# Kernel optimization log

Measured on AMD Instinct MI355X. Metric: run time of the kernel, lower is better.

The kernel has to match this reference:

```python
import jax, jax.numpy as jnp
import numpy as np

TEMPERATURE = 10.0  # module init temperature (training mode)


def setup_inputs() -> dict:
    key = jax.random.key(0)
    kx, kg = jax.random.split(key)
    B, C, H, W = 64, 128, 64, 64
    n = C * H * W  # 524288
    x = jax.random.normal(kx, (B, C, H, W), dtype=jnp.float32)
    # Gumbel(0,1) noise for Gumbel-top-k sampling (== multinomial w/o replacement)
    u = jax.random.uniform(kg, (B, n), dtype=jnp.float32, minval=1e-20, maxval=1.0)
    gumbel = -jnp.log(-jnp.log(u))
    k = int(round(0.1 * n))  # percent_on * n = 52429
    return {"x": x, "gumbel": gumbel, "k": k}


def reference(x, gumbel, k):
    B = x.shape[0]
    n = x.shape[1] * x.shape[2] * x.shape[3]
    flat = x.reshape(B, n)                      # [B, n]
    logits = flat / TEMPERATURE
    # Categorical sampling of k winners without replacement == top-k of
    # gumbel-perturbed logits (equivalent to softmax(logits) + multinomial).
    _, idx = jax.lax.top_k(logits + gumbel, k)  # [B, k]
    mask = jnp.zeros((B, n), dtype=x.dtype).at[jnp.arange(B)[:, None], idx].set(1.0)
    out = (flat * mask).reshape(x.shape)
    return jnp.maximum(out, 0.0)  # relu=True
```

## Files before the change

kernel.cpp:

```cpp
#include <hip/hip_runtime.h>
#include <cstdint>

#define BROWS 64
#define NCOL  524288
#define CHUNKS 32
#define CHUNK  (NCOL / CHUNKS)
#define NV4    (CHUNK / 4)
#define LCAP   2048
#define ECAP   512
#define MAXCAP 24576
#define M_SAMP 32768
#define SEGS   128
#define SBLK   16
#define SLACK  5200
#define HB2    32768

typedef float nf4 __attribute__((ext_vector_type(4)));

#define ABV_OFF   0u
#define CCNT_OFF  256u
#define RINFO_OFF 512u
#define HIST_OFF  4096u
#define CAND_OFF  4096u
#define ZWORDS    (1024 + BROWS * HB2)

__device__ __forceinline__ uint32_t fkey(float s) {
  uint32_t b = __float_as_uint(s);
  return (b & 0x80000000u) ? ~b : (b | 0x80000000u);
}

__global__ __launch_bounds__(256) void k_zero(uint32_t* __restrict__ p, int n) {
  int i = blockIdx.x * 256 + threadIdx.x;
  if (i < n) p[i] = 0;
}

__global__ __launch_bounds__(256) void k_sampleA(const float* __restrict__ x,
                                                 const float* __restrict__ g,
                                                 uint32_t* __restrict__ hist) {
  int row = blockIdx.y;
  size_t rb = (size_t)row * NCOL;
  uint32_t* gh = hist + (size_t)row * HB2;
  int i0 = blockIdx.x * (M_SAMP / SBLK);
  for (int it = 0; it < (M_SAMP / SBLK) / 256; ++it) {
    int i = i0 + it * 256 + threadIdx.x;
    size_t off = rb + (size_t)(i >> 8) * (NCOL / SEGS) + (i & 255);
    uint32_t key = fkey(x[off] / 10.0f + g[off]);
    atomicAdd(&gh[key >> 17], 1u);
  }
}

__global__ __launch_bounds__(256) void k_pick(const uint32_t* __restrict__ hist,
                                              const int* __restrict__ kptr,
                                              uint32_t* __restrict__ rinfo,
                                              uint32_t* __restrict__ abv,
                                              uint32_t* __restrict__ ccnt) {
  __shared__ uint32_t part[256];
  __shared__ uint32_t segbuf[128];
  __shared__ uint32_t sel[4];
  int row = blockIdx.x;
  if (threadIdx.x == 0) { abv[row] = 0; ccnt[row] = 0; }
  const uint32_t* gh = hist + (size_t)row * HB2;
  uint32_t s = 0;
  for (int j = 0; j < HB2 / 256; ++j) s += gh[threadIdx.x * (HB2 / 256) + j];
  part[threadIdx.x] = s;
  __syncthreads();
  if (threadIdx.x == 0) {
    uint32_t kk = (uint32_t)(*kptr);
    uint32_t rHi = ((kk > SLACK ? kk - SLACK : 0u) / 16u) + 1u;
    uint32_t rLo = ((kk + SLACK) / 16u) + 1u;
    if (rLo > M_SAMP) rLo = M_SAMP;
    uint32_t cum = 0, cumHi = 0, cumLo = 0;
    int segHi = -1, segLo = -1;
    for (int t = 255; t >= 0; --t) {
      uint32_t c = part[t];
      if (segHi < 0 && cum + c >= rHi) { segHi = t; cumHi = cum; }
      if (segLo < 0 && cum + c >= rLo) { segLo = t; cumLo = cum; break; }
      cum += c;
    }
    if (segHi < 0) segHi = 0;
    if (segLo < 0) segLo = 0;
    sel[0] = (uint32_t)segHi; sel[1] = rHi - cumHi;
    sel[2] = (uint32_t)segLo; sel[3] = rLo - cumLo;
  }
  __syncthreads();
  int segHi = (int)sel[0], segLo = (int)sel[2];
  if (threadIdx.x < 128) segbuf[threadIdx.x] = gh[segHi * 128 + threadIdx.x];
  __syncthreads();
  if (threadIdx.x == 0) {
    uint32_t rem = sel[1], cum = 0;
    int bin = 0;
    for (int b = 127; b >= 0; --b) {
      uint32_t c = segbuf[b];
      if (cum + c >= rem) { bin = b; break; }
      cum += c;
    }
    uint32_t binHi = (uint32_t)(segHi * 128 + bin);
    rinfo[row * 4 + 0] = (binHi << 17) | 0x1FFFFu;
  }
  __syncthreads();
  if (threadIdx.x < 128) segbuf[threadIdx.x] = gh[segLo * 128 + threadIdx.x];
  __syncthreads();
  if (threadIdx.x == 0) {
    uint32_t rem = sel[3], cum = 0;
    int bin = 0;
    for (int b = 127; b >= 0; --b) {
      uint32_t c = segbuf[b];
      if (cum + c >= rem) { bin = b; break; }
      cum += c;
    }
    uint32_t binLo = (uint32_t)(segLo * 128 + bin);
    rinfo[row * 4 + 1] = binLo << 17;
  }
}

__global__ __launch_bounds__(256) void k_main(const float* __restrict__ x,
                                              const float* __restrict__ g,
                                              const uint32_t* __restrict__ rinfo,
                                              uint64_t* __restrict__ cand,
                                              uint32_t* __restrict__ ccnt,
                                              uint32_t* __restrict__ abv,
                                              float* __restrict__ out, int cap) {
  __shared__ uint64_t lbuf[LCAP];
  __shared__ uint32_t lcnt, lbase;
  __shared__ uint32_t wsum[4];
  int row = blockIdx.y, chunk = blockIdx.x;
  uint32_t keyHi = rinfo[row * 4 + 0];
  uint32_t keyLo = rinfo[row * 4 + 1];
  if (threadIdx.x == 0) lcnt = 0;
  __syncthreads();
  size_t base = (size_t)row * NCOL + (size_t)chunk * CHUNK;
  const float4* x4 = (const float4*)(x + base);
  const float4* g4 = (const float4*)(g + base);
  nf4* o4 = (nf4*)(out + base);
  uint32_t mycnt = 0;
  for (int i = threadIdx.x; i < NV4; i += 256) {
    float4 a = x4[i];
    float4 b = g4[i];
    uint32_t f0 = fkey(a.x / 10.0f + b.x);
    uint32_t f1 = fkey(a.y / 10.0f + b.y);
    uint32_t f2 = fkey(a.z / 10.0f + b.z);
    uint32_t f3 = fkey(a.w / 10.0f + b.w);
    nf4 o;
    o.x = (f0 > keyHi) ? fmaxf(a.x, 0.0f) : 0.0f;
    o.y = (f1 > keyHi) ? fmaxf(a.y, 0.0f) : 0.0f;
    o.z = (f2 > keyHi) ? fmaxf(a.z, 0.0f) : 0.0f;
    o.w = (f3 > keyHi) ? fmaxf(a.w, 0.0f) : 0.0f;
    __builtin_nontemporal_store(o, &o4[i]);
    mycnt += (f0 > keyHi) + (f1 > keyHi) + (f2 > keyHi) + (f3 > keyHi);
    uint32_t li = (uint32_t)(chunk * CHUNK + i * 4);
    if (f0 >= keyLo && f0 <= keyHi) { uint32_t p = atomicAdd(&lcnt, 1u); if (p < LCAP) lbuf[p] = ((uint64_t)f0 << 32) | li; }
    if (f1 >= keyLo && f1 <= keyHi) { uint32_t p = atomicAdd(&lcnt, 1u); if (p < LCAP) lbuf[p] = ((uint64_t)f1 << 32) | (li + 1u); }
    if (f2 >= keyLo && f2 <= keyHi) { uint32_t p = atomicAdd(&lcnt, 1u); if (p < LCAP) lbuf[p] = ((uint64_t)f2 << 32) | (li + 2u); }
    if (f3 >= keyLo && f3 <= keyHi) { uint32_t p = atomicAdd(&lcnt, 1u); if (p < LCAP) lbuf[p] = ((uint64_t)f3 << 32) | (li + 3u); }
  }
  for (int off = 32; off > 0; off >>= 1) mycnt += __shfl_down(mycnt, off);
  int lane = threadIdx.x & 63, wid = threadIdx.x >> 6;
  if (lane == 0) wsum[wid] = mycnt;
  __syncthreads();
  if (threadIdx.x == 0) {
    atomicAdd(&abv[row], wsum[0] + wsum[1] + wsum[2] + wsum[3]);
    lbase = atomicAdd(&ccnt[row], lcnt < LCAP ? lcnt : (uint32_t)LCAP);
  }
  __syncthreads();
  uint32_t cnt = lcnt < LCAP ? lcnt : (uint32_t)LCAP;
  uint64_t* dst = cand + (size_t)row * (size_t)cap;
  for (uint32_t i = threadIdx.x; i < cnt; i += 256) {
    uint32_t p = lbase + i;
    if (p < (uint32_t)cap) dst[p] = lbuf[i];
  }
}

__global__ __launch_bounds__(256) void k_finalize(const float* __restrict__ x,
                                                  const uint64_t* __restrict__ cand,
                                                  const uint32_t* __restrict__ ccnt,
                                                  const uint32_t* __restrict__ abv,
                                                  const uint32_t* __restrict__ rinfo,
                                                  const int* __restrict__ kptr,
                                                  float* __restrict__ out, int cap) {
  __shared__ uint32_t h[4096];
  __shared__ uint32_t part[256];
  __shared__ uint64_t elist[ECAP];
  __shared__ uint32_t ecnt;
  __shared__ int s_cut, s_need2;
  int row = blockIdx.x;
  uint32_t m = ccnt[row];
  if (m > (uint32_t)cap) m = (uint32_t)cap;
  int need = (int)((uint32_t)(*kptr)) - (int)abv[row];
  if (need <= 0) return;
  size_t rb = (size_t)row * NCOL;
  const uint64_t* c = cand + (size_t)row * (size_t)cap;
  if ((uint32_t)need >= m) {
    for (uint32_t i = threadIdx.x; i < m; i += 256) {
      uint32_t idx = (uint32_t)c[i];
      out[rb + idx] = fmaxf(x[rb + idx], 0.0f);
    }
    return;
  }
  uint32_t keyLo = rinfo[row * 4 + 1];
  uint32_t range = rinfo[row * 4 + 0] - keyLo;
  int bits = 32 - __clz((int)(range | 1u));
  int shift = bits > 12 ? bits - 12 : 0;
  for (int i = threadIdx.x; i < 4096; i += 256) h[i] = 0;
  if (threadIdx.x == 0) ecnt = 0;
  __syncthreads();
  for (uint32_t i = threadIdx.x; i < m; i += 256) {
    uint32_t key = (uint32_t)(c[i] >> 32);
    atomicAdd(&h[(key - keyLo) >> shift], 1u);
  }
  __syncthreads();
  uint32_t s = 0;
  for (int j = 0; j < 16; ++j) s += h[threadIdx.x * 16 + j];
  part[threadIdx.x] = s;
  __syncthreads();
  if (threadIdx.x == 0) {
    uint32_t cum = 0;
    int seg = 255;
    for (; seg > 0; --seg) {
      if (cum + part[seg] >= (uint32_t)need) break;
      cum += part[seg];
    }
    int bin = seg * 16 + 15;
    for (; bin > seg * 16; --bin) {
      if (cum + h[bin] >= (uint32_t)need) break;
      cum += h[bin];
    }
    s_cut = bin;
    s_need2 = need - (int)cum;
  }
  __syncthreads();
  int cut = s_cut, need2 = s_need2;
  for (uint32_t i = threadIdx.x; i < m; i += 256) {
    uint64_t e = c[i];
    int bin = (int)(((uint32_t)(e >> 32) - keyLo) >> shift);
    if (bin > cut) {
      uint32_t idx = (uint32_t)e;
      out[rb + idx] = fmaxf(x[rb + idx], 0.0f);
    } else if (bin == cut) {
      uint32_t p = atomicAdd(&ecnt, 1u);
      if (p < ECAP) elist[p] = e ^ 0xFFFFFFFFull;
    }
  }
  __syncthreads();
  int mm = (int)(ecnt < (uint32_t)ECAP ? ecnt : (uint32_t)ECAP);
  for (int pass = 0; pass < mm; ++pass) {
    for (int i = threadIdx.x; 2 * i + (pass & 1) + 1 < mm; i += 256) {
      int a2 = 2 * i + (pass & 1);
      uint64_t va = elist[a2], vb = elist[a2 + 1];
      if (vb > va) { elist[a2] = vb; elist[a2 + 1] = va; }
    }
    __syncthreads();
  }
  int w = need2 < mm ? need2 : mm;
  for (int i = threadIdx.x; i < w; i += 256) {
    uint32_t idx = ~(uint32_t)elist[i];
    out[rb + idx] = fmaxf(x[rb + idx], 0.0f);
  }
}

extern "C" void kernel_launch(void* const* d_in, const int* in_sizes, int n_in,
                              void* d_out, int out_size, void* d_ws, size_t ws_size,
                              hipStream_t stream) {
  const float* x = (const float*)d_in[0];
  const float* g = (const float*)d_in[1];
  const int* kptr = (const int*)d_in[2];
  float* out = (float*)d_out;
  char* ws = (char*)d_ws;

  uint32_t* abv = (uint32_t*)(ws + ABV_OFF);
  uint32_t* ccnt = (uint32_t*)(ws + CCNT_OFF);
  uint32_t* rinfo = (uint32_t*)(ws + RINFO_OFF);
  uint32_t* hist = (uint32_t*)(ws + HIST_OFF);
  uint64_t* cand = (uint64_t*)(ws + CAND_OFF);

  long cap_avail = ((long)ws_size - (long)CAND_OFF) / (8 * BROWS);
  int cap = cap_avail < MAXCAP ? (int)cap_avail : MAXCAP;
  if (cap < 1) cap = 1;

  k_zero<<<(ZWORDS + 255) / 256, 256, 0, stream>>>((uint32_t*)ws, ZWORDS);
  dim3 sgrid(SBLK, BROWS);
  k_sampleA<<<sgrid, 256, 0, stream>>>(x, g, hist);
  k_pick<<<BROWS, 256, 0, stream>>>(hist, kptr, rinfo, abv, ccnt);
  dim3 grid(CHUNKS, BROWS);
  k_main<<<grid, 256, 0, stream>>>(x, g, rinfo, cand, ccnt, abv, out, cap);
  k_finalize<<<BROWS, 256, 0, stream>>>(x, cand, ccnt, abv, rinfo, kptr, out, cap);
}
```

Before: 205.0 us.

## Use per-thread candidate slots, more chunks, prefetch loop, and wider pick kernel

The main kernel splits each row into more chunks. It replaces shared-memory atomic candidate appends with per-thread slot buffers that are compacted through a wave prefix scan, and it software-prefetches the next float4 pair inside a fully unrolled loop. The pick kernel now runs 1024 threads with vectorized histogram reads and finer 32-bin segments. Together these aim to cut LDS atomic contention and raise memory parallelism. The risk is that a thread with more than ten candidates in its small chunk overwrites its last slot and drops candidates.

```diff
diff --git a/kernel.cpp b/kernel.cpp
--- a/kernel.cpp
+++ b/kernel.cpp
@@ -3,10 +3,10 @@
 
 #define BROWS 64
 #define NCOL  524288
-#define CHUNKS 32
+#define CHUNKS 128
 #define CHUNK  (NCOL / CHUNKS)
 #define NV4    (CHUNK / 4)
-#define LCAP   2048
+#define SLOTS  10
 #define ECAP   512
 #define MAXCAP 24576
 #define M_SAMP 32768
@@ -49,19 +49,24 @@
   }
 }
 
-__global__ __launch_bounds__(256) void k_pick(const uint32_t* __restrict__ hist,
-                                              const int* __restrict__ kptr,
-                                              uint32_t* __restrict__ rinfo,
-                                              uint32_t* __restrict__ abv,
-                                              uint32_t* __restrict__ ccnt) {
-  __shared__ uint32_t part[256];
-  __shared__ uint32_t segbuf[128];
+__global__ __launch_bounds__(1024) void k_pick(const uint32_t* __restrict__ hist,
+                                               const int* __restrict__ kptr,
+                                               uint32_t* __restrict__ rinfo,
+                                               uint32_t* __restrict__ abv,
+                                               uint32_t* __restrict__ ccnt) {
+  __shared__ uint32_t part[1024];
+  __shared__ uint32_t segbuf[32];
   __shared__ uint32_t sel[4];
   int row = blockIdx.x;
   if (threadIdx.x == 0) { abv[row] = 0; ccnt[row] = 0; }
   const uint32_t* gh = hist + (size_t)row * HB2;
+  const uint4* gh4 = (const uint4*)gh;
   uint32_t s = 0;
-  for (int j = 0; j < HB2 / 256; ++j) s += gh[threadIdx.x * (HB2 / 256) + j];
+  #pragma unroll
+  for (int j = 0; j < 8; ++j) {
+    uint4 v = gh4[threadIdx.x * 8 + j];
+    s += v.x + v.y + v.z + v.w;
+  }
   part[threadIdx.x] = s;
   __syncthreads();
   if (threadIdx.x == 0) {
@@ -71,7 +76,7 @@
     if (rLo > M_SAMP) rLo = M_SAMP;
     uint32_t cum = 0, cumHi = 0, cumLo = 0;
     int segHi = -1, segLo = -1;
-    for (int t = 255; t >= 0; --t) {
+    for (int t = 1023; t >= 0; --t) {
       uint32_t c = part[t];
       if (segHi < 0 && cum + c >= rHi) { segHi = t; cumHi = cum; }
       if (segLo < 0 && cum + c >= rLo) { segLo = t; cumLo = cum; break; }
@@ -84,31 +89,31 @@
   }
   __syncthreads();
   int segHi = (int)sel[0], segLo = (int)sel[2];
-  if (threadIdx.x < 128) segbuf[threadIdx.x] = gh[segHi * 128 + threadIdx.x];
+  if (threadIdx.x < 32) segbuf[threadIdx.x] = gh[segHi * 32 + threadIdx.x];
   __syncthreads();
   if (threadIdx.x == 0) {
     uint32_t rem = sel[1], cum = 0;
     int bin = 0;
-    for (int b = 127; b >= 0; --b) {
+    for (int b = 31; b >= 0; --b) {
       uint32_t c = segbuf[b];
       if (cum + c >= rem) { bin = b; break; }
       cum += c;
     }
-    uint32_t binHi = (uint32_t)(segHi * 128 + bin);
+    uint32_t binHi = (uint32_t)(segHi * 32 + bin);
     rinfo[row * 4 + 0] = (binHi << 17) | 0x1FFFFu;
   }
   __syncthreads();
-  if (threadIdx.x < 128) segbuf[threadIdx.x] = gh[segLo * 128 + threadIdx.x];
+  if (threadIdx.x < 32) segbuf[threadIdx.x] = gh[segLo * 32 + threadIdx.x];
   __syncthreads();
   if (threadIdx.x == 0) {
     uint32_t rem = sel[3], cum = 0;
     int bin = 0;
-    for (int b = 127; b >= 0; --b) {
+    for (int b = 31; b >= 0; --b) {
       uint32_t c = segbuf[b];
       if (cum + c >= rem) { bin = b; break; }
       cum += c;
     }
-    uint32_t binLo = (uint32_t)(segLo * 128 + bin);
+    uint32_t binLo = (uint32_t)(segLo * 32 + bin);
     rinfo[row * 4 + 1] = binLo << 17;
   }
 }
@@ -120,22 +125,32 @@
                                               uint32_t* __restrict__ ccnt,
                                               uint32_t* __restrict__ abv,
                                               float* __restrict__ out, int cap) {
-  __shared__ uint64_t lbuf[LCAP];
-  __shared__ uint32_t lcnt, lbase;
+  __shared__ uint64_t lbuf[256 * SLOTS];
+  __shared__ uint32_t wpre[4];
   __shared__ uint32_t wsum[4];
+  __shared__ uint32_t lbase;
   int row = blockIdx.y, chunk = blockIdx.x;
   uint32_t keyHi = rinfo[row * 4 + 0];
   uint32_t keyLo = rinfo[row * 4 + 1];
-  if (threadIdx.x == 0) lcnt = 0;
-  __syncthreads();
+  int lane = threadIdx.x & 63, wid = threadIdx.x >> 6;
   size_t base = (size_t)row * NCOL + (size_t)chunk * CHUNK;
   const float4* x4 = (const float4*)(x + base);
   const float4* g4 = (const float4*)(g + base);
   nf4* o4 = (nf4*)(out + base);
+  uint64_t* myslots = &lbuf[(uint32_t)threadIdx.x * SLOTS];
   uint32_t mycnt = 0;
-  for (int i = threadIdx.x; i < NV4; i += 256) {
-    float4 a = x4[i];
-    float4 b = g4[i];
+  uint32_t ccount = 0;
+
+  float4 a = x4[threadIdx.x];
+  float4 b = g4[threadIdx.x];
+  #pragma unroll
+  for (int it = 0; it < NV4 / 256; ++it) {
+    float4 an, bn;
+    if (it < NV4 / 256 - 1) {
+      an = x4[threadIdx.x + (it + 1) * 256];
+      bn = g4[threadIdx.x + (it + 1) * 256];
+    }
+    int idx = it * 256 + threadIdx.x;
     uint32_t f0 = fkey(a.x / 10.0f + b.x);
     uint32_t f1 = fkey(a.y / 10.0f + b.y);
     uint32_t f2 = fkey(a.z / 10.0f + b.z);
@@ -145,28 +160,41 @@
     o.y = (f1 > keyHi) ? fmaxf(a.y, 0.0f) : 0.0f;
     o.z = (f2 > keyHi) ? fmaxf(a.z, 0.0f) : 0.0f;
     o.w = (f3 > keyHi) ? fmaxf(a.w, 0.0f) : 0.0f;
-    __builtin_nontemporal_store(o, &o4[i]);
+    __builtin_nontemporal_store(o, &o4[idx]);
     mycnt += (f0 > keyHi) + (f1 > keyHi) + (f2 > keyHi) + (f3 > keyHi);
-    uint32_t li = (uint32_t)(chunk * CHUNK + i * 4);
-    if (f0 >= keyLo && f0 <= keyHi) { uint32_t p = atomicAdd(&lcnt, 1u); if (p < LCAP) lbuf[p] = ((uint64_t)f0 << 32) | li; }
-    if (f1 >= keyLo && f1 <= keyHi) { uint32_t p = atomicAdd(&lcnt, 1u); if (p < LCAP) lbuf[p] = ((uint64_t)f1 << 32) | (li + 1u); }
-    if (f2 >= keyLo && f2 <= keyHi) { uint32_t p = atomicAdd(&lcnt, 1u); if (p < LCAP) lbuf[p] = ((uint64_t)f2 << 32) | (li + 2u); }
-    if (f3 >= keyLo && f3 <= keyHi) { uint32_t p = atomicAdd(&lcnt, 1u); if (p < LCAP) lbuf[p] = ((uint64_t)f3 << 32) | (li + 3u); }
-  }
-  for (int off = 32; off > 0; off >>= 1) mycnt += __shfl_down(mycnt, off);
-  int lane = threadIdx.x & 63, wid = threadIdx.x >> 6;
-  if (lane == 0) wsum[wid] = mycnt;
-  __syncthreads();
-  if (threadIdx.x == 0) {
+    uint32_t li = (uint32_t)(chunk * CHUNK + idx * 4);
+    if (f0 >= keyLo && f0 <= keyHi) { myslots[ccount < SLOTS ? ccount : SLOTS - 1] = ((uint64_t)f0 << 32) | li;        ccount++; }
+    if (f1 >= keyLo && f1 <= keyHi) { myslots[ccount < SLOTS ? ccount : SLOTS - 1] = ((uint64_t)f1 << 32) | (li + 1u); ccount++; }
+    if (f2 >= keyLo && f2 <= keyHi) { myslots[ccount < SLOTS ? ccount : SLOTS - 1] = ((uint64_t)f2 << 32) | (li + 2u); ccount++; }
+    if (f3 >= keyLo && f3 <= keyHi) { myslots[ccount < SLOTS ? ccount : SLOTS - 1] = ((uint64_t)f3 << 32) | (li + 3u); ccount++; }
+    a = an; b = bn;
+  }
+  uint32_t cstore = ccount < SLOTS ? ccount : SLOTS;
+
+  uint32_t pfx = cstore;
+  #pragma unroll
+  for (int d = 1; d < 64; d <<= 1) {
+    uint32_t t = __shfl_up(pfx, d);
+    if (lane >= d) pfx += t;
+  }
+  uint32_t wtot = __shfl(pfx, 63);
+  if (lane == 63) wpre[wid] = wtot;
+  uint32_t rsum = mycnt;
+  for (int off = 32; off > 0; off >>= 1) rsum += __shfl_down(rsum, off);
+  if (lane == 0) wsum[wid] = rsum;
+  __syncthreads();
+  if (threadIdx.x == 0) {
+    uint32_t t0 = wpre[0], t1 = wpre[1], t2 = wpre[2], t3 = wpre[3];
+    lbase = atomicAdd(&ccnt[row], t0 + t1 + t2 + t3);
+    wpre[0] = 0; wpre[1] = t0; wpre[2] = t0 + t1; wpre[3] = t0 + t1 + t2;
     atomicAdd(&abv[row], wsum[0] + wsum[1] + wsum[2] + wsum[3]);
-    lbase = atomicAdd(&ccnt[row], lcnt < LCAP ? lcnt : (uint32_t)LCAP);
-  }
-  __syncthreads();
-  uint32_t cnt = lcnt < LCAP ? lcnt : (uint32_t)LCAP;
+  }
+  __syncthreads();
+  uint32_t gbase = lbase + wpre[wid] + (pfx - cstore);
   uint64_t* dst = cand + (size_t)row * (size_t)cap;
-  for (uint32_t i = threadIdx.x; i < cnt; i += 256) {
-    uint32_t p = lbase + i;
-    if (p < (uint32_t)cap) dst[p] = lbuf[i];
+  for (uint32_t j = 0; j < cstore; ++j) {
+    uint32_t p = gbase + j;
+    if (p < (uint32_t)cap) dst[p] = myslots[j];
   }
 }
 
@@ -279,7 +307,7 @@
   k_zero<<<(ZWORDS + 255) / 256, 256, 0, stream>>>((uint32_t*)ws, ZWORDS);
   dim3 sgrid(SBLK, BROWS);
   k_sampleA<<<sgrid, 256, 0, stream>>>(x, g, hist);
-  k_pick<<<BROWS, 256, 0, stream>>>(hist, kptr, rinfo, abv, ccnt);
+  k_pick<<<BROWS, 1024, 0, stream>>>(hist, kptr, rinfo, abv, ccnt);
   dim3 grid(CHUNKS, BROWS);
   k_main<<<grid, 256, 0, stream>>>(x, g, rinfo, cand, ccnt, abv, out, cap);
   k_finalize<<<BROWS, 256, 0, stream>>>(x, cand, ccnt, abv, rinfo, kptr, out, cap);
```

After: 240.7 us. 17.4% more time.
